# Performance work log

Measured on AMD Instinct MI355X. Metric: run time of the kernel, lower is better.

The kernel has to match this reference:

```python
import jax, jax.numpy as jnp
import numpy as np

N = 8192          # num nodes
E = 262144        # num edges (avg degree 32)
IN = 128          # in_channels
HID = 64          # hidden_channels
H = 4             # heads (conv1)
OUT = 16          # out_channels
THRESH = 0.5      # distance threshold for adjacency rebuild
SLOPE = 0.2       # PyG GATConv negative_slope default


def setup_inputs() -> dict:
    key = jax.random.key(0)
    ks = jax.random.split(key, 10)
    s = 0.1
    return {
        "x": jax.random.normal(ks[0], (N, IN), jnp.float32),
        "edge_index": jax.random.randint(ks[1], (2, E), 0, N, dtype=jnp.int64),
        # conv1 params (GATConv in->hid, heads=H, concat=True)
        "W1": jax.random.normal(ks[2], (IN, H * HID), jnp.float32) * s,
        "att_src1": jax.random.normal(ks[3], (H, HID), jnp.float32) * s,
        "att_dst1": jax.random.normal(ks[4], (H, HID), jnp.float32) * s,
        "b1": jax.random.normal(ks[5], (H * HID,), jnp.float32) * s,
        # conv2 params (GATConv H*hid->out, heads=1, concat=False)
        "W2": jax.random.normal(ks[6], (H * HID, OUT), jnp.float32) * s,
        "att_src2": jax.random.normal(ks[7], (OUT,), jnp.float32) * s,
        "att_dst2": jax.random.normal(ks[8], (OUT,), jnp.float32) * s,
        "b2": jax.random.normal(ks[9], (OUT,), jnp.float32) * s,
    }


def reference(x, edge_index, W1, att_src1, att_dst1, b1, W2, att_src2, att_dst2, b2):
    n = x.shape[0]
    # ---- conv1: sparse edge-wise GAT (gather -> segment-softmax -> scatter) ----
    h = (x @ W1).reshape(n, H, HID)                         # [N,H,C]
    loops = jnp.arange(n, dtype=edge_index.dtype)           # PyG adds self-loops
    src = jnp.concatenate([edge_index[0], loops])
    dst = jnp.concatenate([edge_index[1], loops])
    a_s = jnp.sum(h * att_src1, axis=-1)                    # [N,H]
    a_d = jnp.sum(h * att_dst1, axis=-1)                    # [N,H]
    e = jax.nn.leaky_relu(a_s[src] + a_d[dst], SLOPE)       # [E+N,H]
    emax = jax.ops.segment_max(e, dst, num_segments=n)      # stable softmax per dst
    ez = jnp.exp(e - emax[dst])
    denom = jax.ops.segment_sum(ez, dst, num_segments=n)
    alpha = ez / denom[dst]                                 # [E+N,H]
    agg = jax.ops.segment_sum(h[src] * alpha[..., None], dst, num_segments=n)
    h1 = jax.nn.elu(agg.reshape(n, H * HID) + b1)           # [N, H*HID]

    # ---- adjacency rebuild: pairwise Euclidean distance + threshold (detached) ----
    f = jax.lax.stop_gradient(h1)                           # torch .detach()
    sq = jnp.sum(f * f, axis=-1)                            # [N]
    d2 = sq[:, None] + sq[None, :] - 2.0 * (f @ f.T)        # squared distances
    dist = jnp.sqrt(jnp.maximum(d2, 0.0))
    adj = dist < THRESH                                     # [N,N], symmetric, self incl.

    # ---- conv2: dense masked GAT attention over rebuilt adjacency (heads=1) ----
    h2 = h1 @ W2                                            # [N,OUT]
    s2 = h2 @ att_src2                                      # [N] (source term)
    t2 = h2 @ att_dst2                                      # [N] (target term)
    # edge j->i exists iff adj[i,j]; score[i,j] = leaky_relu(a_src.h2[j] + a_dst.h2[i])
    scores = jax.nn.leaky_relu(s2[None, :] + t2[:, None], SLOPE)
    scores = jnp.where(adj, scores, -jnp.inf)
    alpha2 = jax.nn.softmax(scores, axis=1)                 # softmax over neighbors j
    out = alpha2 @ h2 + b2                                  # [N,OUT]
    return jax.nn.log_softmax(out, axis=1)
```

## Files before the change

### kernel.cpp

```cpp
#include <hip/hip_runtime.h>
#include <hip/hip_bf16.h>
#include <math.h>

#define NN 8192
#define NE 262144
#define EA (NE + NN)
#define SLOPE 0.2f
#define TH2 0.25f

typedef __bf16 bf16x8 __attribute__((ext_vector_type(8)));
typedef float f32x16 __attribute__((ext_vector_type(16)));

__device__ __forceinline__ float lrelu(float x) { return x > 0.f ? x : SLOPE * x; }

__global__ void k_gemm1(const float* __restrict__ x, const float* __restrict__ W1,
                        const float* __restrict__ as1, const float* __restrict__ ad1,
                        float* __restrict__ h, float* __restrict__ a_s,
                        float* __restrict__ a_d) {
  const int nb = blockIdx.x << 2;
  const int t = threadIdx.x;
  __shared__ float xs[4][128];
  if (t < 128) ((float4*)xs)[t] = ((const float4*)(x + (size_t)nb * 128))[t];
  __syncthreads();
  float ac[4] = {0.f, 0.f, 0.f, 0.f};
  const float* wp = W1 + t;
#pragma unroll 4
  for (int k = 0; k < 128; ++k) {
    float wv = wp[(size_t)k << 8];
    ac[0] = fmaf(xs[0][k], wv, ac[0]);
    ac[1] = fmaf(xs[1][k], wv, ac[1]);
    ac[2] = fmaf(xs[2][k], wv, ac[2]);
    ac[3] = fmaf(xs[3][k], wv, ac[3]);
  }
  const float as1t = as1[t], ad1t = ad1[t];
#pragma unroll
  for (int i = 0; i < 4; ++i) {
    h[((size_t)(nb + i) << 8) + t] = ac[i];
    float av = ac[i] * as1t;
    float dv = ac[i] * ad1t;
#pragma unroll
    for (int m = 32; m >= 1; m >>= 1) {
      av += __shfl_xor(av, m, 64);
      dv += __shfl_xor(dv, m, 64);
    }
    if ((t & 63) == 0) {
      a_s[((nb + i) << 2) + (t >> 6)] = av;
      a_d[((nb + i) << 2) + (t >> 6)] = dv;
    }
  }
}

__global__ void k_init(int* __restrict__ cnt) {
  int i = blockIdx.x * 256 + threadIdx.x;
  if (i < NN) cnt[i] = 1;
}
__global__ void k_hist(const int* __restrict__ ei, int* __restrict__ cnt) {
  int e = blockIdx.x * 256 + threadIdx.x;
  if (e < NE) atomicAdd(&cnt[ei[NE + e]], 1);
}
__global__ void k_scan(const int* __restrict__ cnt, int* __restrict__ start,
                       int* __restrict__ cursor) {
  __shared__ int s[1024];
  const int t = threadIdx.x;
  const int base = t << 3;
  int c[8];
  int run = 0;
#pragma unroll
  for (int i = 0; i < 8; ++i) { c[i] = cnt[base + i]; run += c[i]; }
  s[t] = run;
  __syncthreads();
  const int total = run;
  for (int off = 1; off < 1024; off <<= 1) {
    int v = (t >= off) ? s[t - off] : 0;
    __syncthreads();
    s[t] += v;
    __syncthreads();
  }
  int o = s[t] - total;
#pragma unroll
  for (int i = 0; i < 8; ++i) {
    start[base + i] = o;
    cursor[base + i] = o;
    o += c[i];
  }
}
__global__ void k_scatter(const int* __restrict__ ei, int* __restrict__ cursor,
                          int* __restrict__ eidx) {
  int e = blockIdx.x * 256 + threadIdx.x;
  if (e >= EA) return;
  int src, dst;
  if (e < NE) { src = ei[e]; dst = ei[NE + e]; } else { src = dst = e - NE; }
  int slot = atomicAdd(&cursor[dst], 1);
  eidx[slot] = src;
}

__global__ void k_node(const int* __restrict__ start, const int* __restrict__ cnt,
                       const int* __restrict__ eidx, const float* __restrict__ a_s,
                       const float* __restrict__ a_d, const float* __restrict__ h,
                       const float* __restrict__ b1, const float* __restrict__ W2,
                       const float* __restrict__ as2, const float* __restrict__ ad2,
                       __bf16* __restrict__ fbf, float* __restrict__ sq,
                       float* __restrict__ thr_g, float* __restrict__ s2_g,
                       float* __restrict__ t2g, float* __restrict__ h2g) {
  const int n = blockIdx.x, t = threadIdx.x;
  __shared__ float red[16];
  __shared__ float hl[256];
  __shared__ float r2[4];
  __shared__ float h2l[16];
  const int st = start[n];
  const int deg = cnt[n];
  const float4 ad4 = *(const float4*)(a_d + ((size_t)n << 2));
  float pm0 = -INFINITY, pm1 = -INFINITY, pm2 = -INFINITY, pm3 = -INFINITY;
  for (int e = t; e < deg; e += 256) {
    int src = eidx[st + e];
    float4 s4 = *(const float4*)(a_s + ((size_t)src << 2));
    pm0 = fmaxf(pm0, lrelu(s4.x + ad4.x));
    pm1 = fmaxf(pm1, lrelu(s4.y + ad4.y));
    pm2 = fmaxf(pm2, lrelu(s4.z + ad4.z));
    pm3 = fmaxf(pm3, lrelu(s4.w + ad4.w));
  }
#pragma unroll
  for (int m = 32; m >= 1; m >>= 1) {
    pm0 = fmaxf(pm0, __shfl_xor(pm0, m, 64));
    pm1 = fmaxf(pm1, __shfl_xor(pm1, m, 64));
    pm2 = fmaxf(pm2, __shfl_xor(pm2, m, 64));
    pm3 = fmaxf(pm3, __shfl_xor(pm3, m, 64));
  }
  if ((t & 63) == 0) {
    const int w = t >> 6;
    red[(w << 2) + 0] = pm0;
    red[(w << 2) + 1] = pm1;
    red[(w << 2) + 2] = pm2;
    red[(w << 2) + 3] = pm3;
  }
  __syncthreads();
  const int hd = t >> 6;
  const float mhead = fmaxf(fmaxf(red[0 + hd], red[4 + hd]),
                            fmaxf(red[8 + hd], red[12 + hd]));
  const float adh = (hd == 0) ? ad4.x : (hd == 1) ? ad4.y : (hd == 2) ? ad4.z : ad4.w;
  float dn0 = 0.f, dn1 = 0.f, dn2 = 0.f, dn3 = 0.f;
  float ac0 = 0.f, ac1 = 0.f, ac2 = 0.f, ac3 = 0.f;
  int e = 0;
  for (; e + 3 < deg; e += 4) {
    int s0 = eidx[st + e + 0], s1 = eidx[st + e + 1];
    int s2i = eidx[st + e + 2], s3 = eidx[st + e + 3];
    float z0 = __expf(lrelu(a_s[((size_t)s0 << 2) + hd] + adh) - mhead);
    float z1 = __expf(lrelu(a_s[((size_t)s1 << 2) + hd] + adh) - mhead);
    float z2 = __expf(lrelu(a_s[((size_t)s2i << 2) + hd] + adh) - mhead);
    float z3 = __expf(lrelu(a_s[((size_t)s3 << 2) + hd] + adh) - mhead);
    dn0 += z0; dn1 += z1; dn2 += z2; dn3 += z3;
    ac0 = fmaf(z0, h[((size_t)s0 << 8) + t], ac0);
    ac1 = fmaf(z1, h[((size_t)s1 << 8) + t], ac1);
    ac2 = fmaf(z2, h[((size_t)s2i << 8) + t], ac2);
    ac3 = fmaf(z3, h[((size_t)s3 << 8) + t], ac3);
  }
  for (; e < deg; ++e) {
    int s0 = eidx[st + e];
    float z0 = __expf(lrelu(a_s[((size_t)s0 << 2) + hd] + adh) - mhead);
    dn0 += z0;
    ac0 = fmaf(z0, h[((size_t)s0 << 8) + t], ac0);
  }
  float den = (dn0 + dn1) + (dn2 + dn3);
  float acc = (ac0 + ac1) + (ac2 + ac3);
  float v = acc / den + b1[t];
  float h1 = v > 0.f ? v : (__expf(v) - 1.f);
  fbf[((size_t)n << 8) + t] = (__bf16)h1;
  hl[t] = h1;
  float s = h1 * h1;
#pragma unroll
  for (int m = 32; m >= 1; m >>= 1) s += __shfl_xor(s, m, 64);
  if ((t & 63) == 0) r2[t >> 6] = s;
  __syncthreads();
  if (t < 16) {
    float a = 0.f;
#pragma unroll 8
    for (int c = 0; c < 256; ++c) a = fmaf(hl[c], W2[(c << 4) + t], a);
    h2g[((size_t)n << 4) + t] = a;
    h2l[t] = a;
  }
  __syncthreads();
  if (t == 0) {
    float sqv = r2[0] + r2[1] + r2[2] + r2[3];
    sq[n] = sqv;
    float ss = 0.f;
#pragma unroll
    for (int o = 0; o < 16; ++o) ss += h2l[o] * as2[o];
    thr_g[n] = (sqv - TH2) * 0.5f;
    s2_g[n] = ss;
  } else if (t == 1) {
    float tt = 0.f;
#pragma unroll
    for (int o = 0; o < 16; ++o) tt += h2l[o] * ad2[o];
    t2g[n] = tt;
  }
}

__launch_bounds__(512, 2)
__global__ void k_conv2(const __bf16* __restrict__ fbf, const float* __restrict__ sq,
                        const float* __restrict__ thr_g, const float* __restrict__ s2_g,
                        const float* __restrict__ t2g, const float* __restrict__ h2g,
                        const float* __restrict__ b2, float* __restrict__ out) {
  __shared__ float mrg[512][18];

  const int t = threadIdx.x;
  const int lane = t & 63;
  const int w = t >> 6;
  const int half = lane >> 5;
  const int rowA = lane & 31;
  const int i0 = blockIdx.x << 5;
  const int jw = w << 5;

  bf16x8 bfr[16];
  {
    const char* fb = (const char*)fbf + (((size_t)(i0 + rowA)) << 9) + (half << 4);
#pragma unroll
    for (int kc = 0; kc < 16; ++kc) bfr[kc] = *(const bf16x8*)(fb + kc * 32);
  }
  const float sqi = sq[i0 + rowA];
  const float t2i = t2g[i0 + rowA];
  const float gb_i = 0.5f * sqi;

  float m = -INFINITY, l = 0.f;
  float o[16];
#pragma unroll
  for (int c = 0; c < 16; ++c) o[c] = 0.f;

  for (int jt = 0; jt < 32; ++jt) {
    const int jbase = (jt << 8) + jw;
    bf16x8 afr[16];
    {
      const char* fr = (const char*)fbf + ((size_t)(jbase + rowA) << 9) + (half << 4);
#pragma unroll
      for (int kc = 0; kc < 16; ++kc) afr[kc] = *(const bf16x8*)(fr + kc * 32);
    }
    f32x16 acc0, acc1;
#pragma unroll
    for (int r = 0; r < 16; ++r) { acc0[r] = 0.f; acc1[r] = 0.f; }
#pragma unroll
    for (int kc = 0; kc < 16; kc += 2) {
      acc0 = __builtin_amdgcn_mfma_f32_32x32x16_bf16(afr[kc], bfr[kc], acc0, 0, 0, 0);
      acc1 = __builtin_amdgcn_mfma_f32_32x32x16_bf16(afr[kc + 1], bfr[kc + 1], acc1, 0, 0, 0);
    }

    const float* tb = thr_g + jbase + (half << 2);
    const float* sb = s2_g + jbase + (half << 2);
    float4 thq[4], s2q[4];
#pragma unroll
    for (int q = 0; q < 4; ++q) {
      thq[q] = *(const float4*)(tb + (q << 3));
      s2q[q] = *(const float4*)(sb + (q << 3));
    }
    const float thv[16] = {thq[0].x, thq[0].y, thq[0].z, thq[0].w,
                           thq[1].x, thq[1].y, thq[1].z, thq[1].w,
                           thq[2].x, thq[2].y, thq[2].z, thq[2].w,
                           thq[3].x, thq[3].y, thq[3].z, thq[3].w};
    const float s2v[16] = {s2q[0].x, s2q[0].y, s2q[0].z, s2q[0].w,
                           s2q[1].x, s2q[1].y, s2q[1].z, s2q[1].w,
                           s2q[2].x, s2q[2].y, s2q[2].z, s2q[2].w,
                           s2q[3].x, s2q[3].y, s2q[3].z, s2q[3].w};

    unsigned msk = 0;
#pragma unroll
    for (int r = 0; r < 16; ++r) {
      float g = acc0[r] + acc1[r];
      if (g > gb_i + thv[r]) msk |= (1u << r);
    }

    if (msk) {
      const int j0 = jbase + (half << 2);
#pragma unroll
      for (int r = 0; r < 16; ++r) {
        if (msk & (1u << r)) {
          float e = lrelu(s2v[r] + t2i);
          if (e > m) {
            float scl = __expf(m - e);
            l *= scl;
#pragma unroll
            for (int c = 0; c < 16; ++c) o[c] *= scl;
            m = e;
          }
          float p = __expf(e - m);
          l += p;
          int j = j0 + (r & 3) + ((r >> 2) << 3);
          const float4* hp = (const float4*)(h2g + ((size_t)j << 4));
          float4 q0 = hp[0], q1 = hp[1], q2 = hp[2], q3 = hp[3];
          o[0] += p * q0.x;  o[1] += p * q0.y;  o[2] += p * q0.z;  o[3] += p * q0.w;
          o[4] += p * q1.x;  o[5] += p * q1.y;  o[6] += p * q1.z;  o[7] += p * q1.w;
          o[8] += p * q2.x;  o[9] += p * q2.y;  o[10] += p * q2.z; o[11] += p * q2.w;
          o[12] += p * q3.x; o[13] += p * q3.y; o[14] += p * q3.z; o[15] += p * q3.w;
        }
      }
    }
  }

  {
    float* mp = mrg[(w << 6) + (half << 5) + rowA];
    mp[0] = m;
    mp[1] = l;
#pragma unroll
    for (int c = 0; c < 16; ++c) mp[2 + c] = o[c];
  }
  __syncthreads();
  if (t < 32) {
    float M = -INFINITY;
#pragma unroll
    for (int s = 0; s < 16; ++s)
      M = fmaxf(M, mrg[((s >> 1) << 6) + ((s & 1) << 5) + t][0]);
    float L = 0.f, O[16];
#pragma unroll
    for (int c = 0; c < 16; ++c) O[c] = 0.f;
#pragma unroll
    for (int s = 0; s < 16; ++s) {
      const float* mp = mrg[((s >> 1) << 6) + ((s & 1) << 5) + t];
      float wt = __expf(mp[0] - M);
      L += mp[1] * wt;
#pragma unroll
      for (int c = 0; c < 16; ++c) O[c] += mp[2 + c] * wt;
    }
    float inv = 1.f / L;
    float v[16];
    float mx = -INFINITY;
#pragma unroll
    for (int c = 0; c < 16; ++c) {
      v[c] = O[c] * inv + b2[c];
      mx = fmaxf(mx, v[c]);
    }
    float se = 0.f;
#pragma unroll
    for (int c = 0; c < 16; ++c) se += __expf(v[c] - mx);
    float lse = mx + __logf(se);
    float4* op = (float4*)(out + ((size_t)(i0 + t) << 4));
#pragma unroll
    for (int gq = 0; gq < 4; ++gq)
      op[gq] = make_float4(v[gq * 4 + 0] - lse, v[gq * 4 + 1] - lse,
                           v[gq * 4 + 2] - lse, v[gq * 4 + 3] - lse);
  }
}

extern "C" void kernel_launch(void* const* d_in, const int* in_sizes, int n_in,
                              void* d_out, int out_size, void* d_ws, size_t ws_size,
                              hipStream_t stream) {
  const float* x   = (const float*)d_in[0];
  const int*   ei  = (const int*)d_in[1];
  const float* W1  = (const float*)d_in[2];
  const float* as1 = (const float*)d_in[3];
  const float* ad1 = (const float*)d_in[4];
  const float* b1  = (const float*)d_in[5];
  const float* W2  = (const float*)d_in[6];
  const float* as2 = (const float*)d_in[7];
  const float* ad2 = (const float*)d_in[8];
  const float* b2  = (const float*)d_in[9];
  float* out = (float*)d_out;

  float* p = (float*)d_ws;
  float* h     = p; p += (size_t)NN * 256;
  float* a_s   = p; p += (size_t)NN * 4;
  float* a_d   = p; p += (size_t)NN * 4;
  float* sq    = p; p += NN;
  float* t2    = p; p += NN;
  float* h2g   = p; p += (size_t)NN * 16;
  float* thr_g = p; p += NN;
  float* s2_g  = p; p += NN;
  __bf16* fbf  = (__bf16*)p; p += (size_t)NN * 128;
  int* cnt     = (int*)p; p += NN;
  int* startp  = (int*)p; p += NN;
  int* cursor  = (int*)p; p += NN;
  int* eidx    = (int*)p;

  k_init<<<NN / 256, 256, 0, stream>>>(cnt);
  k_hist<<<NE / 256, 256, 0, stream>>>(ei, cnt);
  k_gemm1<<<NN / 4, 256, 0, stream>>>(x, W1, as1, ad1, h, a_s, a_d);
  k_scan<<<1, 1024, 0, stream>>>(cnt, startp, cursor);
  k_scatter<<<(EA + 255) / 256, 256, 0, stream>>>(ei, cursor, eidx);
  k_node<<<NN, 256, 0, stream>>>(startp, cnt, eidx, a_s, a_d, h, b1, W2, as2, ad2,
                                 fbf, sq, thr_g, s2_g, t2, h2g);
  k_conv2<<<NN / 32, 512, 0, stream>>>(fbf, sq, thr_g, s2_g, t2, h2g, b2, out);
}
```

Measured before the change: 310.6 us.

## Restructure dense conv2 as split-J tiles with async LDS staging and merge kernel

The dense masked-attention kernel is reorganised. Each block now owns 128 query rows and one of eight j-slabs, and the j-tile features are loaded into double-buffered LDS through global_load_lds with an XOR swizzle, so the tile is shared by four waves instead of each wave reading its own rows from global memory. Partial online-softmax states (m, l, o) are written to a workspace, and a new k_merge kernel combines the eight slabs and applies bias and log_softmax. This trades redundant global reads and the per-block LDS merge for an extra launch and partial-state traffic, and it reuses the h buffer as scratch.

```diff
diff --git a/kernel.cpp b/kernel.cpp
--- a/kernel.cpp
+++ b/kernel.cpp
@@ -12,6 +12,11 @@
 typedef float f32x16 __attribute__((ext_vector_type(16)));
 
 __device__ __forceinline__ float lrelu(float x) { return x > 0.f ? x : SLOPE * x; }
+
+__device__ __forceinline__ void gl_lds16(const void* g, void* l) {
+  __builtin_amdgcn_global_load_lds((const __attribute__((address_space(1))) void*)g,
+                                   (__attribute__((address_space(3))) void*)l, 16, 0, 0);
+}
 
 __global__ void k_gemm1(const float* __restrict__ x, const float* __restrict__ W1,
                         const float* __restrict__ as1, const float* __restrict__ ad1,
@@ -195,29 +200,43 @@
   }
 }
 
-__launch_bounds__(512, 2)
+__launch_bounds__(256, 2)
 __global__ void k_conv2(const __bf16* __restrict__ fbf, const float* __restrict__ sq,
                         const float* __restrict__ thr_g, const float* __restrict__ s2_g,
                         const float* __restrict__ t2g, const float* __restrict__ h2g,
-                        const float* __restrict__ b2, float* __restrict__ out) {
-  __shared__ float mrg[512][18];
+                        float* __restrict__ part) {
+  __shared__ __align__(16) char fj[2][16384];
 
   const int t = threadIdx.x;
   const int lane = t & 63;
   const int w = t >> 6;
   const int half = lane >> 5;
-  const int rowA = lane & 31;
-  const int i0 = blockIdx.x << 5;
-  const int jw = w << 5;
+  const int lo = lane & 31;
+  const int ib = blockIdx.x >> 3;
+  const int js = blockIdx.x & 7;
+  const int i0 = ib << 7;
+  const int iw = i0 + (w << 5);
+  const size_t jslab = ((size_t)js << 19);
+
+  int soff[4];
+#pragma unroll
+  for (int p = 0; p < 4; ++p) {
+    int r = (p << 3) + (t >> 5);
+    soff[p] = (r << 9) + (((lo ^ r) & 31) << 4);
+  }
+  int colkey[16];
+#pragma unroll
+  for (int kc = 0; kc < 16; ++kc)
+    colkey[kc] = ((((kc << 1) + half) ^ lo) & 31) << 4;
 
   bf16x8 bfr[16];
   {
-    const char* fb = (const char*)fbf + (((size_t)(i0 + rowA)) << 9) + (half << 4);
+    const char* fb = (const char*)fbf + (((size_t)(iw + lo)) << 9) + (half << 4);
 #pragma unroll
     for (int kc = 0; kc < 16; ++kc) bfr[kc] = *(const bf16x8*)(fb + kc * 32);
   }
-  const float sqi = sq[i0 + rowA];
-  const float t2i = t2g[i0 + rowA];
+  const float sqi = sq[iw + lo];
+  const float t2i = t2g[iw + lo];
   const float gb_i = 0.5f * sqi;
 
   float m = -INFINITY, l = 0.f;
@@ -225,21 +244,31 @@
 #pragma unroll
   for (int c = 0; c < 16; ++c) o[c] = 0.f;
 
+#define STAGE(B, JT)                                                          \
+  do {                                                                        \
+    const char* gsrc = (const char*)fbf + jslab + ((size_t)(JT) << 14);       \
+    _Pragma("unroll") for (int p = 0; p < 4; ++p)                             \
+        gl_lds16(gsrc + soff[p], fj[B] + (p << 12) + (w << 10));              \
+  } while (0)
+
+  STAGE(0, 0);
+  __syncthreads();
+
   for (int jt = 0; jt < 32; ++jt) {
-    const int jbase = (jt << 8) + jw;
-    bf16x8 afr[16];
-    {
-      const char* fr = (const char*)fbf + ((size_t)(jbase + rowA) << 9) + (half << 4);
-#pragma unroll
-      for (int kc = 0; kc < 16; ++kc) afr[kc] = *(const bf16x8*)(fr + kc * 32);
-    }
+    const int cur = jt & 1;
+    if (jt < 31) STAGE(cur ^ 1, jt + 1);
+    const int jbase = (js << 10) + (jt << 5);
+    const char* rb = fj[cur] + (lo << 9);
+
     f32x16 acc0, acc1;
 #pragma unroll
     for (int r = 0; r < 16; ++r) { acc0[r] = 0.f; acc1[r] = 0.f; }
 #pragma unroll
     for (int kc = 0; kc < 16; kc += 2) {
-      acc0 = __builtin_amdgcn_mfma_f32_32x32x16_bf16(afr[kc], bfr[kc], acc0, 0, 0, 0);
-      acc1 = __builtin_amdgcn_mfma_f32_32x32x16_bf16(afr[kc + 1], bfr[kc + 1], acc1, 0, 0, 0);
+      bf16x8 a0 = *(const bf16x8*)(rb + colkey[kc]);
+      bf16x8 a1 = *(const bf16x8*)(rb + colkey[kc + 1]);
+      acc0 = __builtin_amdgcn_mfma_f32_32x32x16_bf16(a0, bfr[kc], acc0, 0, 0, 0);
+      acc1 = __builtin_amdgcn_mfma_f32_32x32x16_bf16(a1, bfr[kc + 1], acc1, 0, 0, 0);
     }
 
     const float* tb = thr_g + jbase + (half << 2);
@@ -291,50 +320,77 @@
         }
       }
     }
-  }
+    __syncthreads();
+  }
+#undef STAGE
 
   {
-    float* mp = mrg[(w << 6) + (half << 5) + rowA];
-    mp[0] = m;
-    mp[1] = l;
-#pragma unroll
-    for (int c = 0; c < 16; ++c) mp[2 + c] = o[c];
-  }
-  __syncthreads();
-  if (t < 32) {
-    float M = -INFINITY;
-#pragma unroll
-    for (int s = 0; s < 16; ++s)
-      M = fmaxf(M, mrg[((s >> 1) << 6) + ((s & 1) << 5) + t][0]);
-    float L = 0.f, O[16];
-#pragma unroll
-    for (int c = 0; c < 16; ++c) O[c] = 0.f;
-#pragma unroll
-    for (int s = 0; s < 16; ++s) {
-      const float* mp = mrg[((s >> 1) << 6) + ((s & 1) << 5) + t];
-      float wt = __expf(mp[0] - M);
-      L += mp[1] * wt;
-#pragma unroll
-      for (int c = 0; c < 16; ++c) O[c] += mp[2 + c] * wt;
-    }
-    float inv = 1.f / L;
-    float v[16];
-    float mx = -INFINITY;
+    float m2 = __shfl_xor(m, 32, 64);
+    float l2 = __shfl_xor(l, 32, 64);
+    float mn = fmaxf(m, m2);
+    float w1 = (m == -INFINITY) ? 0.f : __expf(m - mn);
+    float w2 = (m2 == -INFINITY) ? 0.f : __expf(m2 - mn);
+    l = l * w1 + l2 * w2;
 #pragma unroll
     for (int c = 0; c < 16; ++c) {
-      v[c] = O[c] * inv + b2[c];
-      mx = fmaxf(mx, v[c]);
-    }
-    float se = 0.f;
-#pragma unroll
-    for (int c = 0; c < 16; ++c) se += __expf(v[c] - mx);
-    float lse = mx + __logf(se);
-    float4* op = (float4*)(out + ((size_t)(i0 + t) << 4));
-#pragma unroll
-    for (int gq = 0; gq < 4; ++gq)
-      op[gq] = make_float4(v[gq * 4 + 0] - lse, v[gq * 4 + 1] - lse,
-                           v[gq * 4 + 2] - lse, v[gq * 4 + 3] - lse);
-  }
+      float oc2 = __shfl_xor(o[c], 32, 64);
+      o[c] = o[c] * w1 + oc2 * w2;
+    }
+    m = mn;
+  }
+  if (half == 0) {
+    const int i = iw + lo;
+    part[((size_t)(0 * 8 + js) << 13) + i] = m;
+    part[((size_t)(1 * 8 + js) << 13) + i] = l;
+#pragma unroll
+    for (int c = 0; c < 16; ++c)
+      part[((size_t)((2 + c) * 8 + js) << 13) + i] = o[c];
+  }
+}
+
+__global__ void k_merge(const float* __restrict__ part, const float* __restrict__ b2,
+                        float* __restrict__ out) {
+  const int i = blockIdx.x * 256 + threadIdx.x;
+  float ms[8];
+  float M = -INFINITY;
+#pragma unroll
+  for (int s = 0; s < 8; ++s) {
+    ms[s] = part[((size_t)s << 13) + i];
+    M = fmaxf(M, ms[s]);
+  }
+  float wt[8];
+  float L = 0.f;
+#pragma unroll
+  for (int s = 0; s < 8; ++s) {
+    wt[s] = __expf(ms[s] - M);
+    L += part[((size_t)(8 + s) << 13) + i] * wt[s];
+  }
+  float O[16];
+#pragma unroll
+  for (int c = 0; c < 16; ++c) O[c] = 0.f;
+#pragma unroll
+  for (int s = 0; s < 8; ++s) {
+#pragma unroll
+    for (int c = 0; c < 16; ++c)
+      O[c] += part[((size_t)((2 + c) * 8 + s) << 13) + i] * wt[s];
+  }
+  float inv = 1.f / L;
+  float v[16];
+  float mx = -INFINITY;
+#pragma unroll
+  for (int c = 0; c < 16; ++c) {
+    v[c] = O[c] * inv + b2[c];
+    mx = fmaxf(mx, v[c]);
+  }
+  float se = 0.f;
+#pragma unroll
+  for (int c = 0; c < 16; ++c) se += __expf(v[c] - mx);
+  float lse = mx + __logf(se);
+  float4* op = (float4*)(out + ((size_t)i << 4));
+#pragma unroll
+  for (int gq = 0; gq < 4; ++gq)
+    op[gq] = make_float4(v[gq * 4 + 0] - lse, v[gq * 4 + 1] - lse,
+                         v[gq * 4 + 2] - lse, v[gq * 4 + 3] - lse);
 }
 
 extern "C" void kernel_launch(void* const* d_in, const int* in_sizes, int n_in,
@@ -366,6 +422,7 @@
   int* startp  = (int*)p; p += NN;
   int* cursor  = (int*)p; p += NN;
   int* eidx    = (int*)p;
+  float* part  = h;
 
   k_init<<<NN / 256, 256, 0, stream>>>(cnt);
   k_hist<<<NE / 256, 256, 0, stream>>>(ei, cnt);
@@ -374,5 +431,6 @@
   k_scatter<<<(EA + 255) / 256, 256, 0, stream>>>(ei, cursor, eidx);
   k_node<<<NN, 256, 0, stream>>>(startp, cnt, eidx, a_s, a_d, h, b1, W2, as2, ad2,
                                  fbf, sq, thr_g, s2_g, t2, h2g);
-  k_conv2<<<NN / 32, 512, 0, stream>>>(fbf, sq, thr_g, s2_g, t2, h2g, b2, out);
-}
+  k_conv2<<<512, 256, 0, stream>>>(fbf, sq, thr_g, s2_g, t2, h2g, part);
+  k_merge<<<NN / 256, 256, 0, stream>>>(part, b2, out);
+}
```

After: 250.4 us. 19.4% less time.
